# Kernel tuning notes

Hardware: AMD Instinct MI355X
Metric: run time of the kernel (lower is better)

The kernel has to match this reference:

```python
import jax, jax.numpy as jnp
import numpy as np

D_MODEL = 1024
N_HEADS = 16
HEAD_DIM = D_MODEL // N_HEADS
B, LQ, LK = 4, 2048, 2048


def _rope(x, cos, sin):
    # x: (B, H, L, d); cos/sin: (B, 1, L, d)
    d = x.shape[-1]
    x1, x2 = x[..., : d // 2], x[..., d // 2 :]
    rotated = jnp.concatenate([-x2, x1], axis=-1)
    return x * cos + rotated * sin


def setup_inputs() -> dict:
    key = jax.random.key(0)
    ks = jax.random.split(key, 16)
    s = 1.0 / np.sqrt(D_MODEL)
    inp = {
        "query": jax.random.normal(ks[0], (B, LQ, D_MODEL), jnp.float32),
        "key": jax.random.normal(ks[1], (B, LK, D_MODEL), jnp.float32),
        "value": jax.random.normal(ks[2], (B, LK, D_MODEL), jnp.float32),
        "cos_q": jax.random.normal(ks[3], (B, LQ, HEAD_DIM), jnp.float32),
        "sin_q": jax.random.normal(ks[4], (B, LQ, HEAD_DIM), jnp.float32),
        "cos_k": jax.random.normal(ks[5], (B, LK, HEAD_DIM), jnp.float32),
        "sin_k": jax.random.normal(ks[6], (B, LK, HEAD_DIM), jnp.float32),
        "key_padding_mask": jnp.zeros((B, LK), dtype=bool),
        "Wq": jax.random.normal(ks[7], (D_MODEL, D_MODEL), jnp.float32) * s,
        "bq": jnp.zeros((D_MODEL,), jnp.float32),
        "Wk": jax.random.normal(ks[8], (D_MODEL, D_MODEL), jnp.float32) * s,
        "bk": jnp.zeros((D_MODEL,), jnp.float32),
        "Wv": jax.random.normal(ks[9], (D_MODEL, D_MODEL), jnp.float32) * s,
        "bv": jnp.zeros((D_MODEL,), jnp.float32),
        "Wo": jax.random.normal(ks[10], (D_MODEL, D_MODEL), jnp.float32) * s,
        "bo": jnp.zeros((D_MODEL,), jnp.float32),
    }
    return inp


def reference(query, key, value, cos_q, sin_q, cos_k, sin_k, key_padding_mask,
              Wq, bq, Wk, bk, Wv, bv, Wo, bo):
    Bq, Lq, _ = query.shape
    Lk = key.shape[1]
    scale = HEAD_DIM ** -0.5

    def proj(x, W, b, L):
        # torch Linear: x @ W.T + b, then (B, L, H, d) -> (B, H, L, d)
        y = jnp.einsum('ble,de->bld', x, W) + b
        return y.reshape(Bq, L, N_HEADS, HEAD_DIM).transpose(0, 2, 1, 3)

    q = proj(query, Wq, bq, Lq)
    k = proj(key, Wk, bk, Lk)
    v = proj(value, Wv, bv, Lk)

    q = _rope(q, cos_q[:, None, :Lq, :HEAD_DIM], sin_q[:, None, :Lq, :HEAD_DIM])
    k = _rope(k, cos_k[:, None, :Lk, :HEAD_DIM], sin_k[:, None, :Lk, :HEAD_DIM])

    attn = jnp.einsum('bhqd,bhkd->bhqk', q, k) * scale
    attn = jnp.where(key_padding_mask[:, None, None, :], -jnp.inf, attn)
    attn = jax.nn.softmax(attn, axis=-1)

    out = jnp.einsum('bhqk,bhkd->bhqd', attn, v)
    out = out.transpose(0, 2, 1, 3).reshape(Bq, Lq, D_MODEL)
    return jnp.einsum('ble,de->bld', out, Wo) + bo
```

## Files before the change

kernel.cpp:

```cpp
#include <hip/hip_runtime.h>
#include <hip/hip_bf16.h>
#include <stdint.h>
#include <stddef.h>

#define B_DIM 4
#define NH    16
#define LSEQ  2048
#define HD    64
#define DM    1024
#define TOKENS (B_DIM * LSEQ)

typedef __bf16 bf16_t;
typedef __attribute__((ext_vector_type(8))) __bf16 bf16x8;
typedef __attribute__((ext_vector_type(4))) __bf16 bf16x4;
typedef __attribute__((ext_vector_type(4))) float  f32x4;

#define GLD16(gp, lp) \
  __builtin_amdgcn_global_load_lds((__attribute__((address_space(1))) void*)(gp), \
                                   (__attribute__((address_space(3))) void*)(lp), 16, 0, 0)

__device__ __forceinline__ f32x4 mfma_16x16x32(bf16x8 a, bf16x8 b, f32x4 c) {
  return __builtin_amdgcn_mfma_f32_16x16x32_bf16(a, b, c, 0, 0, 0);
}

__global__ __launch_bounds__(256) void cast3_kernel(const float* __restrict__ a,
                                                    const float* __restrict__ b,
                                                    const float* __restrict__ c,
                                                    bf16_t* __restrict__ dst, int n) {
  const float* src = (blockIdx.y == 0) ? a : (blockIdx.y == 1) ? b : c;
  const int i = (blockIdx.x * 256 + threadIdx.x) * 4;
  if (i < n) {
    const float4 v = *(const float4*)(src + i);
    bf16x4 o;
    o[0] = (bf16_t)v.x; o[1] = (bf16_t)v.y; o[2] = (bf16_t)v.z; o[3] = (bf16_t)v.w;
    *(bf16x4*)(dst + (size_t)blockIdx.y * n + i) = o;
  }
}

__global__ __launch_bounds__(256) void cast4_kernel(const float* __restrict__ a,
                                                    const float* __restrict__ b,
                                                    const float* __restrict__ c,
                                                    const float* __restrict__ d,
                                                    bf16_t* __restrict__ dst, int n) {
  const float* src = (blockIdx.y == 0) ? a : (blockIdx.y == 1) ? b
                   : (blockIdx.y == 2) ? c : d;
  const int i = (blockIdx.x * 256 + threadIdx.x) * 4;
  if (i < n) {
    const float4 v = *(const float4*)(src + i);
    bf16x4 o;
    o[0] = (bf16_t)v.x; o[1] = (bf16_t)v.y; o[2] = (bf16_t)v.z; o[3] = (bf16_t)v.w;
    *(bf16x4*)(dst + (size_t)blockIdx.y * n + i) = o;
  }
}

template <int MODE>
__global__ __launch_bounds__(256) void gemm128_kernel(const bf16_t* __restrict__ A,
                                                      const bf16_t* __restrict__ Bw,
                                                      const float* __restrict__ bias,
                                                      const float* __restrict__ cosb,
                                                      const float* __restrict__ sinb,
                                                      void* __restrict__ outp,
                                                      int M, int N, int K) {
  __shared__ bf16_t As[128 * 32];
  __shared__ bf16_t Bs[128 * 32];
  const int tid  = threadIdx.x;
  const int wave = tid >> 6, lane = tid & 63;
  const int quad = lane >> 4, l16 = lane & 15;
  const int m0 = blockIdx.x * 128, n0 = blockIdx.y * 128;
  const int wm = (wave >> 1) * 64, wn = (wave & 1) * 64;

  f32x4 acc[4][4];
#pragma unroll
  for (int i = 0; i < 4; ++i)
#pragma unroll
    for (int j = 0; j < 4; ++j) acc[i][j] = (f32x4){0.f, 0.f, 0.f, 0.f};

  const int srow = lane >> 2;
  const int scol = (lane & 3) * 8;

  for (int kk = 0; kk < K; kk += 32) {
    __syncthreads();
#pragma unroll
    for (int t = 0; t < 2; ++t) {
      const int c   = wave * 2 + t;
      const int row = c * 16 + srow;
      GLD16(A  + (size_t)(m0 + row) * K + kk + scol, As + c * 512);
      GLD16(Bw + (size_t)(n0 + row) * K + kk + scol, Bs + c * 512);
    }
    __syncthreads();
    bf16x8 af[4], bfr[4];
#pragma unroll
    for (int i = 0; i < 4; ++i)
      af[i] = *(const bf16x8*)(As + (wm + i * 16 + l16) * 32 + quad * 8);
#pragma unroll
    for (int j = 0; j < 4; ++j)
      bfr[j] = *(const bf16x8*)(Bs + (wn + j * 16 + l16) * 32 + quad * 8);
#pragma unroll
    for (int i = 0; i < 4; ++i)
#pragma unroll
      for (int j = 0; j < 4; ++j)
        acc[i][j] = mfma_16x16x32(af[i], bfr[j], acc[i][j]);
  }

  if (MODE == 0) {
    bf16_t* out = (bf16_t*)outp;
    const int h = (n0 + wn) >> 6;
#pragma unroll
    for (int i = 0; i < 4; ++i) {
#pragma unroll
      for (int j = 0; j < 2; ++j) {
        const int hd1 = j * 16 + l16;
        const int hd2 = hd1 + 32;
        const float bn1 = bias[n0 + wn + hd1];
        const float bn2 = bias[n0 + wn + hd2];
#pragma unroll
        for (int r = 0; r < 4; ++r) {
          const int m = m0 + wm + i * 16 + quad * 4 + r;
          const int b = m >> 11, l = m & (LSEQ - 1);
          const size_t cb = ((size_t)b * LSEQ + l) * HD;
          const float x1 = (float)(bf16_t)(acc[i][j][r] + bn1);
          const float x2 = (float)(bf16_t)(acc[i][j + 2][r] + bn2);
          const float c1 = cosb[cb + hd1], s1 = sinb[cb + hd1];
          const float c2 = cosb[cb + hd2], s2 = sinb[cb + hd2];
          bf16_t* dst = out + (((size_t)(b * NH + h)) * LSEQ + l) * HD;
          dst[hd1] = (bf16_t)(x1 * c1 - x2 * s1);
          dst[hd2] = (bf16_t)(x2 * c2 + x1 * s2);
        }
      }
    }
  } else if (MODE == 1) {
    bf16_t* out = (bf16_t*)outp;
#pragma unroll
    for (int i = 0; i < 4; ++i) {
      const int mb = m0 + wm + i * 16 + quad * 4;
      const int b = mb >> 11, l = mb & (LSEQ - 1);
#pragma unroll
      for (int j = 0; j < 4; ++j) {
        const int n = n0 + wn + j * 16 + l16;
        const int h = n >> 6, hd = n & (HD - 1);
        const float bn = bias[n];
        bf16x4 pk;
#pragma unroll
        for (int r = 0; r < 4; ++r) pk[r] = (bf16_t)(acc[i][j][r] + bn);
        *(bf16x4*)(out + (((size_t)(b * NH + h)) * HD + hd) * LSEQ + l) = pk;
      }
    }
  } else {
    float* out = (float*)outp;
#pragma unroll
    for (int i = 0; i < 4; ++i)
#pragma unroll
      for (int j = 0; j < 4; ++j) {
        const int n  = n0 + wn + j * 16 + l16;
        const float bn = bias[n];
#pragma unroll
        for (int r = 0; r < 4; ++r) {
          const int m = m0 + wm + i * 16 + quad * 4 + r;
          out[(size_t)m * N + n] = acc[i][j][r] + bn;
        }
      }
  }
}

__global__ __launch_bounds__(256) void attn_kernel(const bf16_t* __restrict__ qt,
                                                   const bf16_t* __restrict__ kt,
                                                   const bf16_t* __restrict__ vt,
                                                   const unsigned char* __restrict__ mask,
                                                   bf16_t* __restrict__ ctx) {
  __shared__ bf16_t Kl[2 * 64 * 64];
  __shared__ bf16_t Vl[2 * 64 * 64];
  __shared__ bf16_t Pl[4 * 32 * 72];
  const int bh = blockIdx.y;
  const int b = bh >> 4, h = bh & (NH - 1);
  const int q0 = blockIdx.x * 128;
  const int tid = threadIdx.x;
  const int wave = tid >> 6, lane = tid & 63;
  const int quad = lane >> 4, l16 = lane & 15;
  const float scale = 0.125f;

  bf16x8 qa[2][2];
#pragma unroll
  for (int u = 0; u < 2; ++u) {
    const bf16_t* qrow = qt + (((size_t)bh * LSEQ) + q0 + wave * 32 + u * 16 + l16) * HD;
    qa[u][0] = *(const bf16x8*)(qrow + quad * 8);
    qa[u][1] = *(const bf16x8*)(qrow + 32 + quad * 8);
  }

  f32x4 O[2][4];
  float l_part[2][4];
#pragma unroll
  for (int u = 0; u < 2; ++u)
#pragma unroll
    for (int j = 0; j < 4; ++j) { O[u][j] = (f32x4){0.f, 0.f, 0.f, 0.f}; l_part[u][j] = 0.f; }

  const bf16_t* kbase = kt + (size_t)bh * LSEQ * HD;
  const bf16_t* vbase = vt + (size_t)bh * HD * LSEQ;
  const unsigned char* mrow = mask + (size_t)b * LSEQ;

  const int srow = lane >> 3;
  const int scb  = lane & 7;
  bf16_t* Plw = Pl + wave * 32 * 72;

  auto stage = [&](int k0, int buf) {
#pragma unroll
    for (int t = 0; t < 2; ++t) {
      const int c   = wave * 2 + t;
      const int row = c * 8 + srow;
      const int gcb = scb ^ (row & 7);
      GLD16(kbase + (size_t)(k0 + row) * HD + gcb * 8, Kl + buf * 4096 + c * 512);
      GLD16(vbase + (size_t)row * LSEQ + k0 + gcb * 8, Vl + buf * 4096 + c * 512);
    }
  };

  stage(0, 0);

  for (int k0 = 0; k0 < LSEQ; k0 += 64) {
    __syncthreads();
    const int cur = (k0 >> 6) & 1;
    if (k0 + 64 < LSEQ) stage(k0 + 64, cur ^ 1);
    const bf16_t* Kb = Kl + cur * 4096;
    const bf16_t* Vb = Vl + cur * 4096;

    float mb[4];
#pragma unroll
    for (int j = 0; j < 4; ++j)
      mb[j] = mrow[k0 + j * 16 + l16] ? -__builtin_inff() : 0.f;

    f32x4 S[2][4];
#pragma unroll
    for (int j = 0; j < 4; ++j) {
      const int row = j * 16 + l16;
      const int sw  = row & 7;
      const bf16x8 kb0 = *(const bf16x8*)(Kb + row * 64 + ((quad)     ^ sw) * 8);
      const bf16x8 kb1 = *(const bf16x8*)(Kb + row * 64 + ((quad + 4) ^ sw) * 8);
#pragma unroll
      for (int u = 0; u < 2; ++u) {
        f32x4 a = (f32x4){0.f, 0.f, 0.f, 0.f};
        a = mfma_16x16x32(qa[u][0], kb0, a);
        a = mfma_16x16x32(qa[u][1], kb1, a);
#pragma unroll
        for (int r = 0; r < 4; ++r) {
          const float e = __expf(fmaf(a[r], scale, mb[j]));
          S[u][j][r] = e;
          l_part[u][r] += e;
        }
      }
    }

#pragma unroll
    for (int u = 0; u < 2; ++u)
#pragma unroll
      for (int j = 0; j < 4; ++j)
#pragma unroll
        for (int r = 0; r < 4; ++r)
          Plw[(u * 16 + quad * 4 + r) * 72 + j * 16 + l16] = (bf16_t)S[u][j][r];

    bf16x8 pa[2][2];
#pragma unroll
    for (int u = 0; u < 2; ++u) {
      pa[u][0] = *(const bf16x8*)(Plw + (u * 16 + l16) * 72 + quad * 8);
      pa[u][1] = *(const bf16x8*)(Plw + (u * 16 + l16) * 72 + 32 + quad * 8);
    }

#pragma unroll
    for (int jd = 0; jd < 4; ++jd) {
      const int vrow = jd * 16 + l16;
      const int sw   = vrow & 7;
      const bf16x8 vb0 = *(const bf16x8*)(Vb + vrow * 64 + ((quad)     ^ sw) * 8);
      const bf16x8 vb1 = *(const bf16x8*)(Vb + vrow * 64 + ((quad + 4) ^ sw) * 8);
#pragma unroll
      for (int u = 0; u < 2; ++u) {
        O[u][jd] = mfma_16x16x32(pa[u][0], vb0, O[u][jd]);
        O[u][jd] = mfma_16x16x32(pa[u][1], vb1, O[u][jd]);
      }
    }
  }

#pragma unroll
  for (int u = 0; u < 2; ++u)
#pragma unroll
    for (int r = 0; r < 4; ++r) {
      float s = l_part[u][r];
#pragma unroll
      for (int off = 1; off < 16; off <<= 1) s += __shfl_xor(s, off);
      l_part[u][r] = 1.0f / s;
    }

#pragma unroll
  for (int u = 0; u < 2; ++u)
#pragma unroll
    for (int jd = 0; jd < 4; ++jd)
#pragma unroll
      for (int r = 0; r < 4; ++r) {
        const int l = q0 + wave * 32 + u * 16 + quad * 4 + r;
        const int d = h * HD + jd * 16 + l16;
        const float o = O[u][jd][r] * l_part[u][r];
        ctx[((size_t)b * LSEQ + l) * DM + d] = (bf16_t)o;
      }
}

extern "C" void kernel_launch(void* const* d_in, const int* in_sizes, int n_in,
                              void* d_out, int out_size, void* d_ws, size_t ws_size,
                              hipStream_t stream) {
  (void)in_sizes; (void)n_in; (void)out_size; (void)ws_size;
  const float* query = (const float*)d_in[0];
  const float* key   = (const float*)d_in[1];
  const float* value = (const float*)d_in[2];
  const float* cos_q = (const float*)d_in[3];
  const float* sin_q = (const float*)d_in[4];
  const float* cos_k = (const float*)d_in[5];
  const float* sin_k = (const float*)d_in[6];
  const unsigned char* mask = (const unsigned char*)d_in[7];
  const float* Wq = (const float*)d_in[8];
  const float* bq = (const float*)d_in[9];
  const float* Wk = (const float*)d_in[10];
  const float* bk = (const float*)d_in[11];
  const float* Wv = (const float*)d_in[12];
  const float* bv = (const float*)d_in[13];
  const float* Wo = (const float*)d_in[14];
  const float* bo = (const float*)d_in[15];
  float* out = (float*)d_out;

  const size_t ACT = (size_t)TOKENS * DM;
  const size_t WEL = (size_t)DM * DM;

  bf16_t* p   = (bf16_t*)d_ws;
  bf16_t* xq  = p; p += ACT;
  bf16_t* xk  = p; p += ACT;
  bf16_t* xv  = p; p += ACT;
  bf16_t* wqb = p; p += WEL;
  bf16_t* wkb = p; p += WEL;
  bf16_t* wvb = p; p += WEL;
  bf16_t* wob = p; p += WEL;
  bf16_t* qtb = p; p += ACT;
  bf16_t* ktb = p; p += ACT;
  bf16_t* vtb = xq;
  bf16_t* ctx = xk;

  cast3_kernel<<<dim3((int)(ACT / 1024), 3), 256, 0, stream>>>(query, key, value, xq, (int)ACT);
  cast4_kernel<<<dim3((int)(WEL / 1024), 4), 256, 0, stream>>>(Wq, Wk, Wv, Wo, wqb, (int)WEL);

  dim3 gproj(TOKENS / 128, DM / 128);

  gemm128_kernel<0><<<gproj, 256, 0, stream>>>(xq, wqb, bq, cos_q, sin_q, qtb, TOKENS, DM, DM);
  gemm128_kernel<0><<<gproj, 256, 0, stream>>>(xk, wkb, bk, cos_k, sin_k, ktb, TOKENS, DM, DM);
  gemm128_kernel<1><<<gproj, 256, 0, stream>>>(xv, wvb, bv, nullptr, nullptr, vtb, TOKENS, DM, DM);

  attn_kernel<<<dim3(LSEQ / 128, B_DIM * NH), 256, 0, stream>>>(qtb, ktb, vtb, mask, ctx);

  gemm128_kernel<2><<<gproj, 256, 0, stream>>>(ctx, wob, bo, nullptr, nullptr, (void*)out, TOKENS, DM, DM);
}
```

Measured before the change: 426.1 us.

## Batch QKV projections into one launch and simplify attention staging

Merges the three Q/K/V projection GEMMs into a single launch, using blockIdx.z to select input, weight, bias and epilogue. V now gets its own workspace buffer so it no longer aliases xq. The attention kernel drops K/V double buffering in favour of a synchronous single-buffer load per tile, which shrinks shared memory but exposes global load latency. It also switches exp to exp2 with a pre-multiplied log2(e) scale and reuses a smaller per-wave P scratch area one 16-row slice at a time.

```diff
diff --git a/kernel.cpp b/kernel.cpp
--- a/kernel.cpp
+++ b/kernel.cpp
@@ -53,16 +53,25 @@
   }
 }
 
-template <int MODE>
-__global__ __launch_bounds__(256) void gemm128_kernel(const bf16_t* __restrict__ A,
-                                                      const bf16_t* __restrict__ Bw,
-                                                      const float* __restrict__ bias,
-                                                      const float* __restrict__ cosb,
-                                                      const float* __restrict__ sinb,
-                                                      void* __restrict__ outp,
-                                                      int M, int N, int K) {
+__global__ __launch_bounds__(256) void qkv_proj_kernel(const bf16_t* __restrict__ X,
+                                                       const bf16_t* __restrict__ Wb,
+                                                       const float* __restrict__ bq,
+                                                       const float* __restrict__ bk,
+                                                       const float* __restrict__ bv,
+                                                       const float* __restrict__ cos_q,
+                                                       const float* __restrict__ sin_q,
+                                                       const float* __restrict__ cos_k,
+                                                       const float* __restrict__ sin_k,
+                                                       bf16_t* __restrict__ qtb,
+                                                       bf16_t* __restrict__ ktb,
+                                                       bf16_t* __restrict__ vtb) {
   __shared__ bf16_t As[128 * 32];
   __shared__ bf16_t Bs[128 * 32];
+  const int z = blockIdx.z;
+  const bf16_t* A  = X  + (size_t)z * TOKENS * DM;
+  const bf16_t* Bw = Wb + (size_t)z * DM * DM;
+  const float* bias = (z == 0) ? bq : (z == 1) ? bk : bv;
+
   const int tid  = threadIdx.x;
   const int wave = tid >> 6, lane = tid & 63;
   const int quad = lane >> 4, l16 = lane & 15;
@@ -78,14 +87,14 @@
   const int srow = lane >> 2;
   const int scol = (lane & 3) * 8;
 
-  for (int kk = 0; kk < K; kk += 32) {
+  for (int kk = 0; kk < DM; kk += 32) {
     __syncthreads();
 #pragma unroll
     for (int t = 0; t < 2; ++t) {
       const int c   = wave * 2 + t;
       const int row = c * 16 + srow;
-      GLD16(A  + (size_t)(m0 + row) * K + kk + scol, As + c * 512);
-      GLD16(Bw + (size_t)(n0 + row) * K + kk + scol, Bs + c * 512);
+      GLD16(A  + (size_t)(m0 + row) * DM + kk + scol, As + c * 512);
+      GLD16(Bw + (size_t)(n0 + row) * DM + kk + scol, Bs + c * 512);
     }
     __syncthreads();
     bf16x8 af[4], bfr[4];
@@ -102,8 +111,10 @@
         acc[i][j] = mfma_16x16x32(af[i], bfr[j], acc[i][j]);
   }
 
-  if (MODE == 0) {
-    bf16_t* out = (bf16_t*)outp;
+  if (z < 2) {
+    const float* cosb = (z == 0) ? cos_q : cos_k;
+    const float* sinb = (z == 0) ? sin_q : sin_k;
+    bf16_t* out = (z == 0) ? qtb : ktb;
     const int h = (n0 + wn) >> 6;
 #pragma unroll
     for (int i = 0; i < 4; ++i) {
@@ -128,8 +139,7 @@
         }
       }
     }
-  } else if (MODE == 1) {
-    bf16_t* out = (bf16_t*)outp;
+  } else {
 #pragma unroll
     for (int i = 0; i < 4; ++i) {
       const int mb = m0 + wm + i * 16 + quad * 4;
@@ -142,24 +152,69 @@
         bf16x4 pk;
 #pragma unroll
         for (int r = 0; r < 4; ++r) pk[r] = (bf16_t)(acc[i][j][r] + bn);
-        *(bf16x4*)(out + (((size_t)(b * NH + h)) * HD + hd) * LSEQ + l) = pk;
-      }
-    }
-  } else {
-    float* out = (float*)outp;
+        *(bf16x4*)(vtb + (((size_t)(b * NH + h)) * HD + hd) * LSEQ + l) = pk;
+      }
+    }
+  }
+}
+
+__global__ __launch_bounds__(256) void out_gemm_kernel(const bf16_t* __restrict__ A,
+                                                       const bf16_t* __restrict__ Bw,
+                                                       const float* __restrict__ bias,
+                                                       float* __restrict__ out) {
+  __shared__ bf16_t As[128 * 32];
+  __shared__ bf16_t Bs[128 * 32];
+  const int tid  = threadIdx.x;
+  const int wave = tid >> 6, lane = tid & 63;
+  const int quad = lane >> 4, l16 = lane & 15;
+  const int m0 = blockIdx.x * 128, n0 = blockIdx.y * 128;
+  const int wm = (wave >> 1) * 64, wn = (wave & 1) * 64;
+
+  f32x4 acc[4][4];
+#pragma unroll
+  for (int i = 0; i < 4; ++i)
+#pragma unroll
+    for (int j = 0; j < 4; ++j) acc[i][j] = (f32x4){0.f, 0.f, 0.f, 0.f};
+
+  const int srow = lane >> 2;
+  const int scol = (lane & 3) * 8;
+
+  for (int kk = 0; kk < DM; kk += 32) {
+    __syncthreads();
+#pragma unroll
+    for (int t = 0; t < 2; ++t) {
+      const int c   = wave * 2 + t;
+      const int row = c * 16 + srow;
+      GLD16(A  + (size_t)(m0 + row) * DM + kk + scol, As + c * 512);
+      GLD16(Bw + (size_t)(n0 + row) * DM + kk + scol, Bs + c * 512);
+    }
+    __syncthreads();
+    bf16x8 af[4], bfr[4];
 #pragma unroll
     for (int i = 0; i < 4; ++i)
-#pragma unroll
-      for (int j = 0; j < 4; ++j) {
-        const int n  = n0 + wn + j * 16 + l16;
-        const float bn = bias[n];
-#pragma unroll
-        for (int r = 0; r < 4; ++r) {
-          const int m = m0 + wm + i * 16 + quad * 4 + r;
-          out[(size_t)m * N + n] = acc[i][j][r] + bn;
-        }
-      }
-  }
+      af[i] = *(const bf16x8*)(As + (wm + i * 16 + l16) * 32 + quad * 8);
+#pragma unroll
+    for (int j = 0; j < 4; ++j)
+      bfr[j] = *(const bf16x8*)(Bs + (wn + j * 16 + l16) * 32 + quad * 8);
+#pragma unroll
+    for (int i = 0; i < 4; ++i)
+#pragma unroll
+      for (int j = 0; j < 4; ++j)
+        acc[i][j] = mfma_16x16x32(af[i], bfr[j], acc[i][j]);
+  }
+
+#pragma unroll
+  for (int i = 0; i < 4; ++i)
+#pragma unroll
+    for (int j = 0; j < 4; ++j) {
+      const int n  = n0 + wn + j * 16 + l16;
+      const float bn = bias[n];
+#pragma unroll
+      for (int r = 0; r < 4; ++r) {
+        const int m = m0 + wm + i * 16 + quad * 4 + r;
+        out[(size_t)m * DM + n] = acc[i][j][r] + bn;
+      }
+    }
 }
 
 __global__ __launch_bounds__(256) void attn_kernel(const bf16_t* __restrict__ qt,
@@ -167,16 +222,16 @@
                                                    const bf16_t* __restrict__ vt,
                                                    const unsigned char* __restrict__ mask,
                                                    bf16_t* __restrict__ ctx) {
-  __shared__ bf16_t Kl[2 * 64 * 64];
-  __shared__ bf16_t Vl[2 * 64 * 64];
-  __shared__ bf16_t Pl[4 * 32 * 72];
+  __shared__ bf16_t Kl[64 * 64];
+  __shared__ bf16_t Vl[64 * 64];
+  __shared__ bf16_t Pl[4 * 16 * 72];
   const int bh = blockIdx.y;
   const int b = bh >> 4, h = bh & (NH - 1);
   const int q0 = blockIdx.x * 128;
   const int tid = threadIdx.x;
   const int wave = tid >> 6, lane = tid & 63;
   const int quad = lane >> 4, l16 = lane & 15;
-  const float scale = 0.125f;
+  const float scale_l2e = 0.125f * 1.44269504f;
 
   bf16x8 qa[2][2];
 #pragma unroll
@@ -199,27 +254,19 @@
 
   const int srow = lane >> 3;
   const int scb  = lane & 7;
-  bf16_t* Plw = Pl + wave * 32 * 72;
-
-  auto stage = [&](int k0, int buf) {
+  bf16_t* Plw = Pl + wave * 16 * 72;
+
+  for (int k0 = 0; k0 < LSEQ; k0 += 64) {
+    __syncthreads();
 #pragma unroll
     for (int t = 0; t < 2; ++t) {
       const int c   = wave * 2 + t;
       const int row = c * 8 + srow;
       const int gcb = scb ^ (row & 7);
-      GLD16(kbase + (size_t)(k0 + row) * HD + gcb * 8, Kl + buf * 4096 + c * 512);
-      GLD16(vbase + (size_t)row * LSEQ + k0 + gcb * 8, Vl + buf * 4096 + c * 512);
-    }
-  };
-
-  stage(0, 0);
-
-  for (int k0 = 0; k0 < LSEQ; k0 += 64) {
-    __syncthreads();
-    const int cur = (k0 >> 6) & 1;
-    if (k0 + 64 < LSEQ) stage(k0 + 64, cur ^ 1);
-    const bf16_t* Kb = Kl + cur * 4096;
-    const bf16_t* Vb = Vl + cur * 4096;
+      GLD16(kbase + (size_t)(k0 + row) * HD + gcb * 8, Kl + c * 512);
+      GLD16(vbase + (size_t)row * LSEQ + k0 + gcb * 8, Vl + c * 512);
+    }
+    __syncthreads();
 
     float mb[4];
 #pragma unroll
@@ -231,8 +278,8 @@
     for (int j = 0; j < 4; ++j) {
       const int row = j * 16 + l16;
       const int sw  = row & 7;
-      const bf16x8 kb0 = *(const bf16x8*)(Kb + row * 64 + ((quad)     ^ sw) * 8);
-      const bf16x8 kb1 = *(const bf16x8*)(Kb + row * 64 + ((quad + 4) ^ sw) * 8);
+      const bf16x8 kb0 = *(const bf16x8*)(Kl + row * 64 + ((quad)     ^ sw) * 8);
+      const bf16x8 kb1 = *(const bf16x8*)(Kl + row * 64 + ((quad + 4) ^ sw) * 8);
 #pragma unroll
       for (int u = 0; u < 2; ++u) {
         f32x4 a = (f32x4){0.f, 0.f, 0.f, 0.f};
@@ -240,34 +287,31 @@
         a = mfma_16x16x32(qa[u][1], kb1, a);
 #pragma unroll
         for (int r = 0; r < 4; ++r) {
-          const float e = __expf(fmaf(a[r], scale, mb[j]));
+          const float e = __builtin_amdgcn_exp2f(fmaf(a[r], scale_l2e, mb[j]));
           S[u][j][r] = e;
           l_part[u][r] += e;
         }
       }
     }
 
-#pragma unroll
-    for (int u = 0; u < 2; ++u)
+    bf16x8 pa[2][2];
+#pragma unroll
+    for (int u = 0; u < 2; ++u) {
 #pragma unroll
       for (int j = 0; j < 4; ++j)
 #pragma unroll
         for (int r = 0; r < 4; ++r)
-          Plw[(u * 16 + quad * 4 + r) * 72 + j * 16 + l16] = (bf16_t)S[u][j][r];
-
-    bf16x8 pa[2][2];
-#pragma unroll
-    for (int u = 0; u < 2; ++u) {
-      pa[u][0] = *(const bf16x8*)(Plw + (u * 16 + l16) * 72 + quad * 8);
-      pa[u][1] = *(const bf16x8*)(Plw + (u * 16 + l16) * 72 + 32 + quad * 8);
+          Plw[(quad * 4 + r) * 72 + j * 16 + l16] = (bf16_t)S[u][j][r];
+      pa[u][0] = *(const bf16x8*)(Plw + l16 * 72 + quad * 8);
+      pa[u][1] = *(const bf16x8*)(Plw + l16 * 72 + 32 + quad * 8);
     }
 
 #pragma unroll
     for (int jd = 0; jd < 4; ++jd) {
       const int vrow = jd * 16 + l16;
       const int sw   = vrow & 7;
-      const bf16x8 vb0 = *(const bf16x8*)(Vb + vrow * 64 + ((quad)     ^ sw) * 8);
-      const bf16x8 vb1 = *(const bf16x8*)(Vb + vrow * 64 + ((quad + 4) ^ sw) * 8);
+      const bf16x8 vb0 = *(const bf16x8*)(Vl + vrow * 64 + ((quad)     ^ sw) * 8);
+      const bf16x8 vb1 = *(const bf16x8*)(Vl + vrow * 64 + ((quad + 4) ^ sw) * 8);
 #pragma unroll
       for (int u = 0; u < 2; ++u) {
         O[u][jd] = mfma_16x16x32(pa[u][0], vb0, O[u][jd]);
@@ -334,19 +378,17 @@
   bf16_t* wob = p; p += WEL;
   bf16_t* qtb = p; p += ACT;
   bf16_t* ktb = p; p += ACT;
-  bf16_t* vtb = xq;
+  bf16_t* vtb = p; p += ACT;
   bf16_t* ctx = xk;
+  (void)xv; (void)wkb; (void)wvb;
 
   cast3_kernel<<<dim3((int)(ACT / 1024), 3), 256, 0, stream>>>(query, key, value, xq, (int)ACT);
   cast4_kernel<<<dim3((int)(WEL / 1024), 4), 256, 0, stream>>>(Wq, Wk, Wv, Wo, wqb, (int)WEL);
 
-  dim3 gproj(TOKENS / 128, DM / 128);
-
-  gemm128_kernel<0><<<gproj, 256, 0, stream>>>(xq, wqb, bq, cos_q, sin_q, qtb, TOKENS, DM, DM);
-  gemm128_kernel<0><<<gproj, 256, 0, stream>>>(xk, wkb, bk, cos_k, sin_k, ktb, TOKENS, DM, DM);
-  gemm128_kernel<1><<<gproj, 256, 0, stream>>>(xv, wvb, bv, nullptr, nullptr, vtb, TOKENS, DM, DM);
+  qkv_proj_kernel<<<dim3(TOKENS / 128, DM / 128, 3), 256, 0, stream>>>(
+      xq, wqb, bq, bk, bv, cos_q, sin_q, cos_k, sin_k, qtb, ktb, vtb);
 
   attn_kernel<<<dim3(LSEQ / 128, B_DIM * NH), 256, 0, stream>>>(qtb, ktb, vtb, mask, ctx);
 
-  gemm128_kernel<2><<<gproj, 256, 0, stream>>>(ctx, wob, bo, nullptr, nullptr, (void*)out, TOKENS, DM, DM);
-}
+  out_gemm_kernel<<<dim3(TOKENS / 128, DM / 128), 256, 0, stream>>>(ctx, wob, bo, out);
+}
```

New measurement: 391.1 us. 8.2% less time.
